# Performance work log

Hardware: AMD Instinct MI355X
Metric: run time of the kernel (lower is better)

## Reference

```python
import jax, jax.numpy as jnp
import numpy as np

B, NPG = 128, 512            # graphs, nodes per graph (batch is contiguous & uniform)
N = B * NPG                  # 65536 nodes
DEG = 8
E = N * DEG                  # 524288 edges
F_IN, NHID = 128, 64
H, C = 3, NHID               # GAT heads, out channels per head
HC = H * C                   # 192
NCLS = 10
RATIO = 0.5
NEG_SLOPE = 0.2


def setup_inputs() -> dict:
    key = jax.random.key(0)
    ks = jax.random.split(key, 24)
    x = jax.random.normal(ks[0], (N, F_IN), jnp.float32)
    # edges constrained within each graph (graphs are contiguous blocks of NPG nodes)
    offs = jnp.repeat(jnp.arange(B, dtype=jnp.int32) * NPG, NPG * DEG)
    src = jax.random.randint(ks[1], (E,), 0, NPG, dtype=jnp.int32) + offs
    dst = jax.random.randint(ks[2], (E,), 0, NPG, dtype=jnp.int32) + offs
    edge_index = jnp.stack([src, dst], axis=0)
    edge_attr = jax.random.normal(ks[3], (E, 2), jnp.float32)
    batch = jnp.repeat(jnp.arange(B, dtype=jnp.int32), NPG)

    def lin(k, o, i):
        return jax.random.normal(k, (o, i), jnp.float32) / np.float32(np.sqrt(i))

    return {
        "x": x, "edge_index": edge_index, "edge_attr": edge_attr, "batch": batch,
        # lin: num_features -> nhid//2
        "W_lin": lin(ks[4], NHID // 2, F_IN), "b_lin": jnp.zeros((NHID // 2,), jnp.float32),
        # GATConv(nhid//2 -> nhid, heads=3, edge_dim=2)
        "W_src": lin(ks[5], HC, NHID // 2),
        "att_src": jax.random.normal(ks[6], (H, C), jnp.float32) / np.float32(np.sqrt(C)),
        "att_dst": jax.random.normal(ks[7], (H, C), jnp.float32) / np.float32(np.sqrt(C)),
        "W_edge": lin(ks[8], HC, 2),
        "att_edge": jax.random.normal(ks[9], (H, C), jnp.float32) / np.float32(np.sqrt(C)),
        "b_gat": jnp.zeros((HC,), jnp.float32),
        # SAGPool score layer: GCNConv(nhid*3 -> 1)
        "W_gcn": lin(ks[10], 1, HC), "b_gcn": jnp.zeros((1,), jnp.float32),
        # classifier MLP
        "W1": lin(ks[11], NHID, 2 * HC), "b1": jnp.zeros((NHID,), jnp.float32),
        "W2": lin(ks[12], NHID // 2, NHID), "b2": jnp.zeros((NHID // 2,), jnp.float32),
        "W3": lin(ks[13], NCLS, NHID // 2), "b3": jnp.zeros((NCLS,), jnp.float32),
    }


def reference(x, edge_index, edge_attr, batch,
              W_lin, b_lin, W_src, att_src, att_dst, W_edge, att_edge, b_gat,
              W_gcn, b_gcn, W1, b1, W2, b2, W3, b3):
    src, dst = edge_index[0], edge_index[1]

    # ---- lin + ELU -------------------------------------------------------
    h = jax.nn.elu(x @ W_lin.T + b_lin)                       # [N, nhid//2]

    # ---- GATConv(heads=3, edge_dim=2), add_self_loops fill_value='mean' --
    loop = jnp.arange(N, dtype=src.dtype)
    cnt = jax.ops.segment_sum(jnp.ones((E,), h.dtype), dst, num_segments=N)
    loop_attr = jax.ops.segment_sum(edge_attr, dst, num_segments=N) / jnp.maximum(cnt, 1.0)[:, None]
    s_full = jnp.concatenate([src, loop])
    d_full = jnp.concatenate([dst, loop])
    ea_full = jnp.concatenate([edge_attr, loop_attr], axis=0)  # [E+N, 2]

    xp = (h @ W_src.T).reshape(N, H, C)                        # projected per-head feats
    a_src = (xp * att_src).sum(-1)                             # [N, H]
    a_dst = (xp * att_dst).sum(-1)                             # [N, H]
    ef = (ea_full @ W_edge.T).reshape(-1, H, C)
    a_edge = (ef * att_edge).sum(-1)                           # [E+N, H]

    alpha = jax.nn.leaky_relu(a_src[s_full] + a_dst[d_full] + a_edge, NEG_SLOPE)
    m = jax.ops.segment_max(alpha, d_full, num_segments=N)     # scatter-softmax over dst
    ealpha = jnp.exp(alpha - m[d_full])
    denom = jax.ops.segment_sum(ealpha, d_full, num_segments=N)
    alpha = ealpha / (denom[d_full] + 1e-16)                   # [E+N, H]

    out = jax.ops.segment_sum(alpha[:, :, None] * xp[s_full], d_full, num_segments=N)
    x1 = jax.nn.relu(out.reshape(N, HC) + b_gat)               # [N, 192]

    # ---- SAGPool: GCNConv score + per-graph top-k (mask form) ------------
    xw = x1 @ W_gcn.T                                          # [N, 1]
    deg = jax.ops.segment_sum(jnp.ones((E,), x1.dtype), dst, num_segments=N) + 1.0
    dinv = jax.lax.rsqrt(deg)
    agg = jax.ops.segment_sum((dinv[src] * dinv[dst])[:, None] * xw[src], dst, num_segments=N)
    score = (agg + (dinv ** 2)[:, None] * xw + b_gcn)[:, 0]    # [N]

    k = int(np.ceil(RATIO * NPG))                              # nodes kept per graph
    s2 = score.reshape(B, NPG)
    rank = jnp.argsort(jnp.argsort(-s2, axis=1), axis=1)
    mask = rank < k                                            # [B, NPG] top-k selection

    xs = (x1 * jnp.tanh(score)[:, None]).reshape(B, NPG, HC)
    gmp = jnp.max(jnp.where(mask[:, :, None], xs, -jnp.inf), axis=1)   # [B, 192]
    gap = jnp.sum(jnp.where(mask[:, :, None], xs, 0.0), axis=1) / k    # [B, 192]
    r = jnp.concatenate([gmp, gap], axis=1)                    # [B, 384]

    # ---- classifier MLP (dropout is identity in eval) ---------------------
    r = jax.nn.relu(r @ W1.T + b1)
    r = jax.nn.relu(r @ W2.T + b2)
    return jax.nn.log_softmax(r @ W3.T + b3, axis=-1)          # [B, num_classes]
```

## Files before the change

kernel.cpp:

```cpp
#include <hip/hip_runtime.h>
#include <hip/hip_bf16.h>
#include <math.h>

#define NN   65536
#define EE   524288
#define BB   128
#define NPGC 512
#define HCC  192
#define KSEL 256
#define NEG  0.2f
#define PSEG 8
#define SEGN (NPGC / PSEG)
#define MAXD 40
#define SLOTS ((size_t)NN * MAXD)
#define EPG   4096

__device__ __forceinline__ int nodeblock_base(int bx) {
    int xcd = bx & 7, j = bx >> 3;
    int g = xcd + 8 * (j >> 1);
    return g * NPGC + (j & 1) * 256;
}

__global__ __launch_bounds__(256) void k_h(
    const float* __restrict__ x, const float* __restrict__ W_lin,
    const float* __restrict__ b_lin, float* __restrict__ hbuf) {
    __shared__ float Wl[128 * 16];
    int t = threadIdx.x;
    int half = blockIdx.y;
#pragma unroll
    for (int i = 0; i < 8; ++i) {
        int idx = t + i * 256;
        int k = idx >> 4, jj = idx & 15;
        Wl[idx] = W_lin[(half * 16 + jj) * 128 + k];
    }
    __syncthreads();
    int n = nodeblock_base(blockIdx.x) + t;
    const float4* xr = (const float4*)(x + (size_t)n * 128);
    float acc[16];
#pragma unroll
    for (int j = 0; j < 16; ++j) acc[j] = b_lin[half * 16 + j];
#pragma unroll 4
    for (int q = 0; q < 32; ++q) {
        float4 a = xr[q];
        const float* w = &Wl[(q * 4) * 16];
#pragma unroll
        for (int j = 0; j < 16; ++j) {
            acc[j] += a.x * w[j] + a.y * w[16 + j] +
                      a.z * w[32 + j] + a.w * w[48 + j];
        }
    }
#pragma unroll
    for (int j = 0; j < 16; ++j)
        acc[j] = acc[j] > 0.f ? acc[j] : expm1f(acc[j]);
    float4* dst = (float4*)(hbuf + (size_t)n * 32 + half * 16);
#pragma unroll
    for (int q = 0; q < 4; ++q)
        dst[q] = make_float4(acc[4 * q], acc[4 * q + 1],
                             acc[4 * q + 2], acc[4 * q + 3]);
}

__global__ __launch_bounds__(256) void k_xp(
    const float* __restrict__ hbuf, const float* __restrict__ W_src,
    const float* __restrict__ att_src, const float* __restrict__ att_dst,
    float* __restrict__ xp, float* __restrict__ ap_s, float* __restrict__ ap_d) {
    __shared__ float Ws[32 * 33];
    int t = threadIdx.x;
    int h = blockIdx.y;
    int ch = blockIdx.z;
    {
        int rowbase = (h * 64 + ch * 32) * 32;
#pragma unroll
        for (int i = 0; i < 4; ++i) {
            int idx = t + i * 256;
            int r = idx >> 5, k = idx & 31;
            Ws[k * 33 + r] = W_src[rowbase + idx];
        }
    }
    __syncthreads();
    int n = nodeblock_base(blockIdx.x) + t;
    const float4* hr = (const float4*)(hbuf + (size_t)n * 32);
    float acc[32];
#pragma unroll
    for (int c = 0; c < 32; ++c) acc[c] = 0.f;
#pragma unroll
    for (int q = 0; q < 8; ++q) {
        float4 hv = hr[q];
        const float* w = &Ws[(q * 4) * 33];
#pragma unroll
        for (int c = 0; c < 32; ++c) {
            acc[c] += hv.x * w[c] + hv.y * w[33 + c] +
                      hv.z * w[66 + c] + hv.w * w[99 + c];
        }
    }
    float as = 0.f, ad = 0.f;
    const float* ats = att_src + h * 64 + ch * 32;
    const float* atd = att_dst + h * 64 + ch * 32;
#pragma unroll
    for (int c = 0; c < 32; ++c) {
        as += acc[c] * ats[c];
        ad += acc[c] * atd[c];
    }
    ap_s[(size_t)(ch * 3 + h) * NN + n] = as;
    ap_d[(size_t)(ch * 3 + h) * NN + n] = ad;
    float4* dst = (float4*)(xp + (size_t)n * HCC + h * 64 + ch * 32);
#pragma unroll
    for (int q = 0; q < 8; ++q)
        dst[q] = make_float4(acc[4 * q], acc[4 * q + 1],
                             acc[4 * q + 2], acc[4 * q + 3]);
}

__global__ __launch_bounds__(1024) void k_edges(
    const int* __restrict__ ei, const float* __restrict__ ea,
    const float* __restrict__ ap_s, const float* __restrict__ ap_d,
    const float* __restrict__ W_edge, const float* __restrict__ att_edge,
    int* __restrict__ fill, float4* __restrict__ slotA) {
    __shared__ int   s_pos[NPGC];
    __shared__ float s_la[NPGC * 2];
    __shared__ float s_as[NPGC * 3], s_ad[NPGC * 3];
    __shared__ float s_ac[6];
    int b = blockIdx.x, t = threadIdx.x;
    int g = (b & 7) + 8 * (b >> 3);
    int nbase = g * NPGC;
    int ebase = g * EPG;
    if (t < NPGC) s_pos[t] = 0;
    s_la[t] = 0.f;
    if (t < 6) s_ac[t] = 0.f;
    for (int i = t; i < NPGC * 3; i += 1024) {
        int h = i >> 9, nl = i & (NPGC - 1);
        s_as[nl * 3 + h] = ap_s[(size_t)h * NN + nbase + nl] +
                           ap_s[(size_t)(3 + h) * NN + nbase + nl];
        s_ad[nl * 3 + h] = ap_d[(size_t)h * NN + nbase + nl] +
                           ap_d[(size_t)(3 + h) * NN + nbase + nl];
    }
    __syncthreads();
    if (t < 192) {
        float ae = att_edge[t];
        int h = t >> 6;
        atomicAdd(&s_ac[h],     W_edge[2 * t]     * ae);
        atomicAdd(&s_ac[3 + h], W_edge[2 * t + 1] * ae);
    }
    int4  se  = ((const int4*)(ei + ebase))[t];
    int4  de  = ((const int4*)(ei + EE + ebase))[t];
    float4 a0 = ((const float4*)(ea + 2 * ebase))[2 * t];
    float4 a1 = ((const float4*)(ea + 2 * ebase))[2 * t + 1];
    __syncthreads();
    float ac[6];
#pragma unroll
    for (int h = 0; h < 6; ++h) ac[h] = s_ac[h];

    int   ss[4] = {se.x, se.y, se.z, se.w};
    int   dd[4] = {de.x, de.y, de.z, de.w};
    float e0v[4] = {a0.x, a0.z, a1.x, a1.z};
    float e1v[4] = {a0.y, a0.w, a1.y, a1.w};
#pragma unroll
    for (int k = 0; k < 4; ++k) {
        int s = ss[k], d = dd[k];
        int sl = s & (NPGC - 1), dl = d & (NPGC - 1);
        float e0 = e0v[k], e1 = e1v[k];
        atomicAdd(&s_la[2 * dl],     e0);
        atomicAdd(&s_la[2 * dl + 1], e1);
        float v[3];
#pragma unroll
        for (int h = 0; h < 3; ++h) {
            float a = s_as[sl * 3 + h] + s_ad[dl * 3 + h] +
                      e0 * ac[h] + e1 * ac[3 + h];
            v[h] = a >= 0.f ? a : NEG * a;
        }
        int pos = atomicAdd(&s_pos[dl], 1);
        if (pos < MAXD - 1)
            slotA[(size_t)(nbase + dl) * MAXD + 1 + pos] =
                make_float4(v[0], v[1], v[2], __int_as_float(s));
    }
    __syncthreads();
    if (t < NPGC) {
        int cnt = s_pos[t];
        int n = nbase + t;
        fill[n] = cnt;
        float inv = 1.f / fmaxf((float)cnt, 1.f);
        float l0 = s_la[2 * t] * inv, l1 = s_la[2 * t + 1] * inv;
        float v[3];
#pragma unroll
        for (int h = 0; h < 3; ++h) {
            float a = s_as[t * 3 + h] + s_ad[t * 3 + h] +
                      l0 * ac[h] + l1 * ac[3 + h];
            v[h] = a >= 0.f ? a : NEG * a;
        }
        slotA[(size_t)n * MAXD] = make_float4(v[0], v[1], v[2],
                                              __int_as_float(n));
    }
}

__global__ __launch_bounds__(256) void k_agg(
    const int* __restrict__ fill, const float4* __restrict__ slotA,
    const float* __restrict__ xp,
    const float* __restrict__ b_gat, const float* __restrict__ W_gcn,
    float* __restrict__ x1, float* __restrict__ xwd, float* __restrict__ dinv) {
    __shared__ float2 wsl[4][3][64];
    int wave = threadIdx.x >> 6, lane = threadIdx.x & 63;
    int b = blockIdx.x;
    int xcd = b & 7, j = b >> 3;
    int g = (j >> 7) * 8 + xcd;
    int n = g * NPGC + (j & 127) * 4 + wave;

    int ctrue = fill[n];
    int cnt = ctrue < (MAXD - 1) ? ctrue : (MAXD - 1);
    int tot = cnt + 1;

    if (lane < tot) {
        float4 pk = slotA[(size_t)n * MAXD + lane];
        wsl[wave][0][lane] = make_float2(__expf(pk.x), pk.w);
        wsl[wave][1][lane] = make_float2(__expf(pk.y), pk.w);
        wsl[wave][2][lane] = make_float2(__expf(pk.z), pk.w);
    }
    bool act = lane < 48;
    int head = act ? (lane >> 4) : 0;
    const float2* wp = wsl[wave][head];
    const float4* xp4 = (const float4*)xp;
    float ax = 0.f, ay = 0.f, az = 0.f, aw = 0.f, den = 0.f;
    int s = 0;
    for (; s + 3 < tot; s += 4) {
        float2 wsA = wp[s],     wsB = wp[s + 1];
        float2 wsC = wp[s + 2], wsD = wp[s + 3];
        den += (wsA.x + wsB.x) + (wsC.x + wsD.x);
        if (act) {
            float4 vA = xp4[(size_t)__float_as_int(wsA.y) * 48 + lane];
            float4 vB = xp4[(size_t)__float_as_int(wsB.y) * 48 + lane];
            float4 vC = xp4[(size_t)__float_as_int(wsC.y) * 48 + lane];
            float4 vD = xp4[(size_t)__float_as_int(wsD.y) * 48 + lane];
            ax += wsA.x * vA.x + wsB.x * vB.x + wsC.x * vC.x + wsD.x * vD.x;
            ay += wsA.x * vA.y + wsB.x * vB.y + wsC.x * vC.y + wsD.x * vD.y;
            az += wsA.x * vA.z + wsB.x * vB.z + wsC.x * vC.z + wsD.x * vD.z;
            aw += wsA.x * vA.w + wsB.x * vB.w + wsC.x * vC.w + wsD.x * vD.w;
        }
    }
    for (; s < tot; ++s) {
        float2 wsA = wp[s];
        den += wsA.x;
        if (act) {
            float4 vA = xp4[(size_t)__float_as_int(wsA.y) * 48 + lane];
            ax += wsA.x * vA.x; ay += wsA.x * vA.y;
            az += wsA.x * vA.z; aw += wsA.x * vA.w;
        }
    }
    float p = 0.f;
    if (act) {
        float id = 1.f / (den + 1e-16f);
        float4 bg = ((const float4*)b_gat)[lane];
        float4 v;
        v.x = fmaxf(ax * id + bg.x, 0.f);
        v.y = fmaxf(ay * id + bg.y, 0.f);
        v.z = fmaxf(az * id + bg.z, 0.f);
        v.w = fmaxf(aw * id + bg.w, 0.f);
        ((float4*)x1)[(size_t)n * 48 + lane] = v;
        float4 wg = ((const float4*)W_gcn)[lane];
        p = v.x * wg.x + v.y * wg.y + v.z * wg.z + v.w * wg.w;
    }
#pragma unroll
    for (int msk = 32; msk > 0; msk >>= 1) p += __shfl_xor(p, msk, 64);
    if (lane == 0) {
        float dv = rsqrtf((float)ctrue + 1.f);
        xwd[n] = p * dv;
        dinv[n] = dv;
    }
}

__global__ __launch_bounds__(256) void k_score(
    const int* __restrict__ fill, const float4* __restrict__ slotA,
    const float* __restrict__ xwd, const float* __restrict__ dinv,
    const float* __restrict__ b_gcn, float* __restrict__ score) {
    int wave = threadIdx.x >> 6, lane = threadIdx.x & 63;
    int b = blockIdx.x;
    int xcd = b & 7, j = b >> 3;
    int g = (j >> 7) * 8 + xcd;
    int n = g * NPGC + (j & 127) * 4 + wave;

    int ctrue = fill[n];
    int cnt = ctrue < (MAXD - 1) ? ctrue : (MAXD - 1);
    float acc = 0.f;
    if (lane <= cnt) {
        int src = __float_as_int(
            ((const float*)slotA)[((size_t)n * MAXD + lane) * 4 + 3]);
        acc = xwd[src];
    }
#pragma unroll
    for (int msk = 32; msk > 0; msk >>= 1) acc += __shfl_xor(acc, msk, 64);
    if (lane == 0) score[n] = b_gcn[0] + dinv[n] * acc;
}

__global__ __launch_bounds__(192) void k_poolrank(
    const float* __restrict__ score, const float* __restrict__ x1,
    float* __restrict__ pmax, float* __restrict__ psum) {
    __shared__ float sc[NPGC];
    __shared__ float ts_s[SEGN];
    __shared__ int sel_s[SEGN];
    int b = blockIdx.x;
    int xcd = b & 7, gslot = (b >> 3) & 15, seg = b >> 7;
    int g = gslot * 8 + xcd;
    int t = threadIdx.x;
    int gbase = g * NPGC;
    for (int i = t; i < NPGC; i += 192) sc[i] = score[gbase + i];
    __syncthreads();
    if (t < SEGN) {
        int iloc = seg * SEGN + t;
        float si = sc[iloc];
        int rank = 0;
        for (int j = 0; j < NPGC; ++j) {
            float sj = sc[j];
            rank += (sj > si) || (sj == si && j < iloc);
        }
        sel_s[t] = (rank < KSEL) ? 1 : 0;
        ts_s[t] = tanhf(si);
    }
    __syncthreads();
    int nb = gbase + seg * SEGN;
    float mx = -1e30f, sm = 0.f;
    for (int i = 0; i < SEGN; ++i) {
        if (sel_s[i]) {
            float v = x1[(size_t)(nb + i) * HCC + t] * ts_s[i];
            mx = fmaxf(mx, v);
            sm += v;
        }
    }
    size_t pb = (size_t)(g * PSEG + seg) * HCC + t;
    pmax[pb] = mx;
    psum[pb] = sm;
}

__global__ __launch_bounds__(384) void k_mlp(
    const float* __restrict__ pmax, const float* __restrict__ psum,
    const float* __restrict__ W1, const float* __restrict__ b1,
    const float* __restrict__ W2, const float* __restrict__ b2,
    const float* __restrict__ W3, const float* __restrict__ b3,
    float* __restrict__ out) {
    __shared__ float rs[384], part[384], h1[64], h2[32], lg[10], mls;
    int g = blockIdx.x, t = threadIdx.x;
    if (t < HCC) {
        float mx = -1e30f, sm = 0.f;
#pragma unroll
        for (int s = 0; s < PSEG; ++s) {
            mx = fmaxf(mx, pmax[(size_t)(g * PSEG + s) * HCC + t]);
            sm += psum[(size_t)(g * PSEG + s) * HCC + t];
        }
        rs[t] = mx;
        rs[HCC + t] = sm * (1.f / (float)KSEL);
    }
    __syncthreads();
    {
        int o = t / 6, sl = t - o * 6;
        const float* wr = W1 + o * 384 + sl * 64;
        const float* rr = rs + sl * 64;
        float s = 0.f;
#pragma unroll 8
        for (int k = 0; k < 64; ++k) s += rr[k] * wr[k];
        part[t] = s;
    }
    __syncthreads();
    if (t < 64) {
        float s = b1[t];
#pragma unroll
        for (int j = 0; j < 6; ++j) s += part[t * 6 + j];
        h1[t] = fmaxf(s, 0.f);
    }
    __syncthreads();
    if (t < 256) {
        int o = t >> 3, sl = t & 7;
        const float* wr = W2 + o * 64 + sl * 8;
        const float* hr = h1 + sl * 8;
        float s = 0.f;
#pragma unroll
        for (int k = 0; k < 8; ++k) s += hr[k] * wr[k];
        part[t] = s;
    }
    __syncthreads();
    if (t < 32) {
        float s = b2[t];
#pragma unroll
        for (int j = 0; j < 8; ++j) s += part[t * 8 + j];
        h2[t] = fmaxf(s, 0.f);
    }
    __syncthreads();
    if (t < 10) {
        float s = b3[t];
        for (int k = 0; k < 32; ++k) s += h2[k] * W3[t * 32 + k];
        lg[t] = s;
    }
    __syncthreads();
    if (t == 0) {
        float mx = lg[0];
        for (int j = 1; j < 10; ++j) mx = fmaxf(mx, lg[j]);
        float se = 0.f;
        for (int j = 0; j < 10; ++j) se += expf(lg[j] - mx);
        mls = mx + logf(se);
    }
    __syncthreads();
    if (t < 10) out[g * 10 + t] = lg[t] - mls;
}

extern "C" void kernel_launch(void* const* d_in, const int* in_sizes, int n_in,
                              void* d_out, int out_size, void* d_ws, size_t ws_size,
                              hipStream_t stream) {
    const float* x        = (const float*)d_in[0];
    const int*   ei       = (const int*)d_in[1];
    const float* ea       = (const float*)d_in[2];
    const float* W_lin    = (const float*)d_in[4];
    const float* b_lin    = (const float*)d_in[5];
    const float* W_src    = (const float*)d_in[6];
    const float* att_src  = (const float*)d_in[7];
    const float* att_dst  = (const float*)d_in[8];
    const float* W_edge   = (const float*)d_in[9];
    const float* att_edge = (const float*)d_in[10];
    const float* b_gat    = (const float*)d_in[11];
    const float* W_gcn    = (const float*)d_in[12];
    const float* b_gcn    = (const float*)d_in[13];
    const float* W1 = (const float*)d_in[14]; const float* b1 = (const float*)d_in[15];
    const float* W2 = (const float*)d_in[16]; const float* b2 = (const float*)d_in[17];
    const float* W3 = (const float*)d_in[18]; const float* b3 = (const float*)d_in[19];
    float* out = (float*)d_out;

    char* ws = (char*)d_ws;
    size_t off = 0;
    auto alloc = [&](size_t bytes) {
        size_t r = off;
        off += (bytes + 255) & ~(size_t)255;
        return r;
    };
    float* xp      = (float*)(ws + alloc((size_t)NN * HCC * 4));
    float* x1      = (float*)(ws + alloc((size_t)NN * HCC * 4));
    float* hbuf    = (float*)(ws + alloc((size_t)NN * 32 * 4));
    int*   fill    = (int*)(ws + alloc((size_t)NN * 4));
    float* ap_s    = (float*)(ws + alloc((size_t)NN * 6 * 4));
    float* ap_d    = (float*)(ws + alloc((size_t)NN * 6 * 4));
    float4* slotA  = (float4*)(ws + alloc(SLOTS * 16));
    float* xwd     = (float*)(ws + alloc((size_t)NN * 4));
    float* dinv    = (float*)(ws + alloc((size_t)NN * 4));
    float* score   = (float*)(ws + alloc((size_t)NN * 4));
    float* pmax    = (float*)(ws + alloc((size_t)BB * PSEG * HCC * 4));
    float* psum    = (float*)(ws + alloc((size_t)BB * PSEG * HCC * 4));

    k_h<<<dim3(256, 2), 256, 0, stream>>>(x, W_lin, b_lin, hbuf);
    k_xp<<<dim3(256, 3, 2), 256, 0, stream>>>(hbuf, W_src, att_src, att_dst,
                                              xp, ap_s, ap_d);
    k_edges<<<BB, 1024, 0, stream>>>(ei, ea, ap_s, ap_d, W_edge, att_edge,
                                     fill, slotA);
    k_agg<<<NN / 4, 256, 0, stream>>>(fill, slotA, xp, b_gat, W_gcn,
                                      x1, xwd, dinv);
    k_score<<<NN / 4, 256, 0, stream>>>(fill, slotA, xwd, dinv, b_gcn, score);
    k_poolrank<<<BB * PSEG, 192, 0, stream>>>(score, x1, pmax, psum);
    k_mlp<<<BB, 384, 0, stream>>>(pmax, psum, W1, b1, W2, b2, W3, b3, out);
}
```

Before: 262.1 us.

## Fold attention vectors into W_src and compute alpha logits in first linear kernel

A tiny new kernel precomputes W_src^T·att_src/att_dst per head and the edge-attention coefficients once. k_h then computes the per-node attention logits directly from the hidden features, and now processes two nodes per thread. k_xp is restructured to keep W_src rows in registers and stage hbuf in shared memory, so one block covers all three heads. k_edges drops its redundant per-block reduction. This removes the 3x2 grid replication of k_xp and the logit dot products at the cost of one extra launch and higher register pressure.

```diff
diff --git a/kernel.cpp b/kernel.cpp
--- a/kernel.cpp
+++ b/kernel.cpp
@@ -21,110 +21,168 @@
     return g * NPGC + (j & 1) * 256;
 }
 
+__global__ __launch_bounds__(192) void k_v(
+    const float* __restrict__ W_src, const float* __restrict__ att_src,
+    const float* __restrict__ att_dst, const float* __restrict__ W_edge,
+    const float* __restrict__ att_edge, float* __restrict__ vbuf) {
+    __shared__ float red[6];
+    int t = threadIdx.x;
+    if (t < 6) red[t] = 0.f;
+    __syncthreads();
+    {
+        float ae = att_edge[t];
+        int h = t >> 6;
+        atomicAdd(&red[h],     W_edge[2 * t]     * ae);
+        atomicAdd(&red[3 + h], W_edge[2 * t + 1] * ae);
+    }
+    if (t < 96) {
+        int h = t >> 5, k = t & 31;
+        float vs = 0.f, vd = 0.f;
+        for (int c = 0; c < 64; ++c) {
+            float w = W_src[(h * 64 + c) * 32 + k];
+            vs += w * att_src[h * 64 + c];
+            vd += w * att_dst[h * 64 + c];
+        }
+        vbuf[t] = vs;
+        vbuf[96 + t] = vd;
+    }
+    __syncthreads();
+    if (t < 6) vbuf[192 + t] = red[t];
+}
+
 __global__ __launch_bounds__(256) void k_h(
     const float* __restrict__ x, const float* __restrict__ W_lin,
-    const float* __restrict__ b_lin, float* __restrict__ hbuf) {
+    const float* __restrict__ b_lin, const float* __restrict__ vbuf,
+    float* __restrict__ hbuf, float* __restrict__ ap_s, float* __restrict__ ap_d) {
     __shared__ float Wl[128 * 16];
+    __shared__ float vs_s[48], vd_s[48];
     int t = threadIdx.x;
     int half = blockIdx.y;
 #pragma unroll
     for (int i = 0; i < 8; ++i) {
         int idx = t + i * 256;
         int k = idx >> 4, jj = idx & 15;
-        Wl[idx] = W_lin[(half * 16 + jj) * 128 + k];
-    }
-    __syncthreads();
-    int n = nodeblock_base(blockIdx.x) + t;
-    const float4* xr = (const float4*)(x + (size_t)n * 128);
-    float acc[16];
-#pragma unroll
-    for (int j = 0; j < 16; ++j) acc[j] = b_lin[half * 16 + j];
-#pragma unroll 4
+        Wl[k * 16 + jj] = W_lin[(half * 16 + jj) * 128 + k];
+    }
+    if (t < 48) {
+        int head = t >> 4, j = t & 15;
+        vs_s[t] = vbuf[head * 32 + half * 16 + j];
+        vd_s[t] = vbuf[96 + head * 32 + half * 16 + j];
+    }
+    __syncthreads();
+    int g = (blockIdx.x & 7) + 8 * (blockIdx.x >> 3);
+    int nA = g * NPGC + t, nB = nA + 256;
+    const float4* xrA = (const float4*)(x + (size_t)nA * 128);
+    const float4* xrB = (const float4*)(x + (size_t)nB * 128);
+    float accA[16], accB[16];
+#pragma unroll
+    for (int j = 0; j < 16; ++j) {
+        float bv = b_lin[half * 16 + j];
+        accA[j] = bv; accB[j] = bv;
+    }
+#pragma unroll 2
     for (int q = 0; q < 32; ++q) {
-        float4 a = xr[q];
-        const float* w = &Wl[(q * 4) * 16];
+        float4 xA = xrA[q], xB = xrB[q];
+        const float4* w0 = (const float4*)&Wl[(q * 4 + 0) * 16];
+        const float4* w1 = (const float4*)&Wl[(q * 4 + 1) * 16];
+        const float4* w2 = (const float4*)&Wl[(q * 4 + 2) * 16];
+        const float4* w3 = (const float4*)&Wl[(q * 4 + 3) * 16];
+#pragma unroll
+        for (int jq = 0; jq < 4; ++jq) {
+            float4 a = w0[jq], b = w1[jq], c = w2[jq], d = w3[jq];
+            accA[4*jq+0] += xA.x*a.x + xA.y*b.x + xA.z*c.x + xA.w*d.x;
+            accA[4*jq+1] += xA.x*a.y + xA.y*b.y + xA.z*c.y + xA.w*d.y;
+            accA[4*jq+2] += xA.x*a.z + xA.y*b.z + xA.z*c.z + xA.w*d.z;
+            accA[4*jq+3] += xA.x*a.w + xA.y*b.w + xA.z*c.w + xA.w*d.w;
+            accB[4*jq+0] += xB.x*a.x + xB.y*b.x + xB.z*c.x + xB.w*d.x;
+            accB[4*jq+1] += xB.x*a.y + xB.y*b.y + xB.z*c.y + xB.w*d.y;
+            accB[4*jq+2] += xB.x*a.z + xB.y*b.z + xB.z*c.z + xB.w*d.z;
+            accB[4*jq+3] += xB.x*a.w + xB.y*b.w + xB.z*c.w + xB.w*d.w;
+        }
+    }
+#pragma unroll
+    for (int j = 0; j < 16; ++j) {
+        accA[j] = accA[j] > 0.f ? accA[j] : expm1f(accA[j]);
+        accB[j] = accB[j] > 0.f ? accB[j] : expm1f(accB[j]);
+    }
+    float4* dA = (float4*)(hbuf + (size_t)nA * 32 + half * 16);
+    float4* dB = (float4*)(hbuf + (size_t)nB * 32 + half * 16);
+#pragma unroll
+    for (int q = 0; q < 4; ++q) {
+        dA[q] = make_float4(accA[4*q], accA[4*q+1], accA[4*q+2], accA[4*q+3]);
+        dB[q] = make_float4(accB[4*q], accB[4*q+1], accB[4*q+2], accB[4*q+3]);
+    }
+#pragma unroll
+    for (int head = 0; head < 3; ++head) {
+        float sA = 0.f, dAv = 0.f, sB = 0.f, dBv = 0.f;
 #pragma unroll
         for (int j = 0; j < 16; ++j) {
-            acc[j] += a.x * w[j] + a.y * w[16 + j] +
-                      a.z * w[32 + j] + a.w * w[48 + j];
-        }
-    }
-#pragma unroll
-    for (int j = 0; j < 16; ++j)
-        acc[j] = acc[j] > 0.f ? acc[j] : expm1f(acc[j]);
-    float4* dst = (float4*)(hbuf + (size_t)n * 32 + half * 16);
-#pragma unroll
-    for (int q = 0; q < 4; ++q)
-        dst[q] = make_float4(acc[4 * q], acc[4 * q + 1],
-                             acc[4 * q + 2], acc[4 * q + 3]);
+            sA  += accA[j] * vs_s[head * 16 + j];
+            dAv += accA[j] * vd_s[head * 16 + j];
+            sB  += accB[j] * vs_s[head * 16 + j];
+            dBv += accB[j] * vd_s[head * 16 + j];
+        }
+        size_t pb = (size_t)(half * 3 + head) * NN;
+        ap_s[pb + nA] = sA;  ap_s[pb + nB] = sB;
+        ap_d[pb + nA] = dAv; ap_d[pb + nB] = dBv;
+    }
 }
 
 __global__ __launch_bounds__(256) void k_xp(
     const float* __restrict__ hbuf, const float* __restrict__ W_src,
-    const float* __restrict__ att_src, const float* __restrict__ att_dst,
-    float* __restrict__ xp, float* __restrict__ ap_s, float* __restrict__ ap_d) {
-    __shared__ float Ws[32 * 33];
+    float* __restrict__ xp) {
+    __shared__ float hs[256 * 32];
     int t = threadIdx.x;
-    int h = blockIdx.y;
-    int ch = blockIdx.z;
-    {
-        int rowbase = (h * 64 + ch * 32) * 32;
-#pragma unroll
-        for (int i = 0; i < 4; ++i) {
-            int idx = t + i * 256;
-            int r = idx >> 5, k = idx & 31;
-            Ws[k * 33 + r] = W_src[rowbase + idx];
-        }
-    }
-    __syncthreads();
-    int n = nodeblock_base(blockIdx.x) + t;
-    const float4* hr = (const float4*)(hbuf + (size_t)n * 32);
-    float acc[32];
-#pragma unroll
-    for (int c = 0; c < 32; ++c) acc[c] = 0.f;
-#pragma unroll
-    for (int q = 0; q < 8; ++q) {
-        float4 hv = hr[q];
-        const float* w = &Ws[(q * 4) * 33];
-#pragma unroll
-        for (int c = 0; c < 32; ++c) {
-            acc[c] += hv.x * w[c] + hv.y * w[33 + c] +
-                      hv.z * w[66 + c] + hv.w * w[99 + c];
-        }
-    }
-    float as = 0.f, ad = 0.f;
-    const float* ats = att_src + h * 64 + ch * 32;
-    const float* atd = att_dst + h * 64 + ch * 32;
-#pragma unroll
-    for (int c = 0; c < 32; ++c) {
-        as += acc[c] * ats[c];
-        ad += acc[c] * atd[c];
-    }
-    ap_s[(size_t)(ch * 3 + h) * NN + n] = as;
-    ap_d[(size_t)(ch * 3 + h) * NN + n] = ad;
-    float4* dst = (float4*)(xp + (size_t)n * HCC + h * 64 + ch * 32);
-#pragma unroll
-    for (int q = 0; q < 8; ++q)
-        dst[q] = make_float4(acc[4 * q], acc[4 * q + 1],
-                             acc[4 * q + 2], acc[4 * q + 3]);
+    int nb = nodeblock_base(blockIdx.x);
+    for (int i = t; i < 256 * 32; i += 256) hs[i] = hbuf[(size_t)nb * 32 + i];
+    int lane = t & 63, wave = t >> 6;
+    float wreg[96];
+#pragma unroll
+    for (int h = 0; h < 3; ++h) {
+        const float4* wp = (const float4*)(W_src + (h * 64 + lane) * 32);
+#pragma unroll
+        for (int q = 0; q < 8; ++q) {
+            float4 w = wp[q];
+            wreg[h * 32 + 4 * q]     = w.x;
+            wreg[h * 32 + 4 * q + 1] = w.y;
+            wreg[h * 32 + 4 * q + 2] = w.z;
+            wreg[h * 32 + 4 * q + 3] = w.w;
+        }
+    }
+    __syncthreads();
+    int n0 = wave * 64;
+    for (int nd = 0; nd < 64; ++nd) {
+        int nl = n0 + nd;
+        const float4* hr = (const float4*)&hs[nl * 32];
+        float a0 = 0.f, a1 = 0.f, a2 = 0.f;
+#pragma unroll
+        for (int q = 0; q < 8; ++q) {
+            float4 hv = hr[q];
+            a0 += hv.x*wreg[4*q] + hv.y*wreg[4*q+1] + hv.z*wreg[4*q+2] + hv.w*wreg[4*q+3];
+            a1 += hv.x*wreg[32+4*q] + hv.y*wreg[32+4*q+1] + hv.z*wreg[32+4*q+2] + hv.w*wreg[32+4*q+3];
+            a2 += hv.x*wreg[64+4*q] + hv.y*wreg[64+4*q+1] + hv.z*wreg[64+4*q+2] + hv.w*wreg[64+4*q+3];
+        }
+        size_t nbase = (size_t)(nb + nl) * HCC;
+        xp[nbase + lane] = a0;
+        xp[nbase + 64 + lane] = a1;
+        xp[nbase + 128 + lane] = a2;
+    }
 }
 
 __global__ __launch_bounds__(1024) void k_edges(
     const int* __restrict__ ei, const float* __restrict__ ea,
     const float* __restrict__ ap_s, const float* __restrict__ ap_d,
-    const float* __restrict__ W_edge, const float* __restrict__ att_edge,
+    const float* __restrict__ vbuf,
     int* __restrict__ fill, float4* __restrict__ slotA) {
     __shared__ int   s_pos[NPGC];
     __shared__ float s_la[NPGC * 2];
     __shared__ float s_as[NPGC * 3], s_ad[NPGC * 3];
-    __shared__ float s_ac[6];
     int b = blockIdx.x, t = threadIdx.x;
     int g = (b & 7) + 8 * (b >> 3);
     int nbase = g * NPGC;
     int ebase = g * EPG;
     if (t < NPGC) s_pos[t] = 0;
     s_la[t] = 0.f;
-    if (t < 6) s_ac[t] = 0.f;
     for (int i = t; i < NPGC * 3; i += 1024) {
         int h = i >> 9, nl = i & (NPGC - 1);
         s_as[nl * 3 + h] = ap_s[(size_t)h * NN + nbase + nl] +
@@ -132,21 +190,14 @@
         s_ad[nl * 3 + h] = ap_d[(size_t)h * NN + nbase + nl] +
                            ap_d[(size_t)(3 + h) * NN + nbase + nl];
     }
-    __syncthreads();
-    if (t < 192) {
-        float ae = att_edge[t];
-        int h = t >> 6;
-        atomicAdd(&s_ac[h],     W_edge[2 * t]     * ae);
-        atomicAdd(&s_ac[3 + h], W_edge[2 * t + 1] * ae);
-    }
+    float ac[6];
+#pragma unroll
+    for (int h = 0; h < 6; ++h) ac[h] = vbuf[192 + h];
     int4  se  = ((const int4*)(ei + ebase))[t];
     int4  de  = ((const int4*)(ei + EE + ebase))[t];
     float4 a0 = ((const float4*)(ea + 2 * ebase))[2 * t];
     float4 a1 = ((const float4*)(ea + 2 * ebase))[2 * t + 1];
     __syncthreads();
-    float ac[6];
-#pragma unroll
-    for (int h = 0; h < 6; ++h) ac[h] = s_ac[h];
 
     int   ss[4] = {se.x, se.y, se.z, se.w};
     int   dd[4] = {de.x, de.y, de.z, de.w};
@@ -195,7 +246,7 @@
     const float* __restrict__ xp,
     const float* __restrict__ b_gat, const float* __restrict__ W_gcn,
     float* __restrict__ x1, float* __restrict__ xwd, float* __restrict__ dinv) {
-    __shared__ float2 wsl[4][3][64];
+    __shared__ float2 wsl[4][3][65];
     int wave = threadIdx.x >> 6, lane = threadIdx.x & 63;
     int b = blockIdx.x;
     int xcd = b & 7, j = b >> 3;
@@ -214,7 +265,7 @@
     }
     bool act = lane < 48;
     int head = act ? (lane >> 4) : 0;
-    const float2* wp = wsl[wave][head];
+    const float2* wp = &wsl[wave][head][0];
     const float4* xp4 = (const float4*)xp;
     float ax = 0.f, ay = 0.f, az = 0.f, aw = 0.f, den = 0.f;
     int s = 0;
@@ -434,14 +485,15 @@
     float* xwd     = (float*)(ws + alloc((size_t)NN * 4));
     float* dinv    = (float*)(ws + alloc((size_t)NN * 4));
     float* score   = (float*)(ws + alloc((size_t)NN * 4));
+    float* vbuf    = (float*)(ws + alloc(256 * 4));
     float* pmax    = (float*)(ws + alloc((size_t)BB * PSEG * HCC * 4));
     float* psum    = (float*)(ws + alloc((size_t)BB * PSEG * HCC * 4));
 
-    k_h<<<dim3(256, 2), 256, 0, stream>>>(x, W_lin, b_lin, hbuf);
-    k_xp<<<dim3(256, 3, 2), 256, 0, stream>>>(hbuf, W_src, att_src, att_dst,
-                                              xp, ap_s, ap_d);
-    k_edges<<<BB, 1024, 0, stream>>>(ei, ea, ap_s, ap_d, W_edge, att_edge,
-                                     fill, slotA);
+    k_v<<<1, 192, 0, stream>>>(W_src, att_src, att_dst, W_edge, att_edge, vbuf);
+    k_h<<<dim3(128, 2), 256, 0, stream>>>(x, W_lin, b_lin, vbuf,
+                                          hbuf, ap_s, ap_d);
+    k_xp<<<256, 256, 0, stream>>>(hbuf, W_src, xp);
+    k_edges<<<BB, 1024, 0, stream>>>(ei, ea, ap_s, ap_d, vbuf, fill, slotA);
     k_agg<<<NN / 4, 256, 0, stream>>>(fill, slotA, xp, b_gat, W_gcn,
                                       x1, xwd, dinv);
     k_score<<<NN / 4, 256, 0, stream>>>(fill, slotA, xwd, dinv, b_gcn, score);
```

Result: no change. 263.7 us (+0.6%).
